# Optimization experiments

Measured on AMD Instinct MI355X. Metric: run time of the kernel, lower is better.

The kernel has to match this reference:

```python
import jax, jax.numpy as jnp
import numpy as np

B, D, N = 2, 512, 2048
H, K, V = 8, 64, 64


def setup_inputs() -> dict:
    key = jax.random.key(0)
    ks = jax.random.split(key, 5)
    scale = 0.02
    return {
        "x": jax.random.normal(ks[0], (B, D, N), dtype=jnp.float32),
        "query_proj": jax.random.normal(ks[1], (H, K, D), dtype=jnp.float32) * scale,
        "key_proj": jax.random.normal(ks[2], (D, K), dtype=jnp.float32) * scale,
        "value_proj": jax.random.normal(ks[3], (D, V), dtype=jnp.float32) * scale,
        "output_proj": jax.random.normal(ks[4], (D, H, V), dtype=jnp.float32) * scale,
    }


def reference(x, query_proj, key_proj, value_proj, output_proj):
    # x: (b, d, n); self-attention, so memory m = x as well
    key_dim = query_proj.shape[1]
    q = jnp.einsum('bdn,hkd->bnhk', x, query_proj)          # (b,n,h,k)
    k = jnp.einsum('bdm,dk->bmk', x, key_proj)              # (b,m,k) shared across heads
    v = jnp.einsum('bdm,dv->bmv', x, value_proj)            # (b,m,v) shared across heads
    sim = jnp.einsum('bnhk,bmk->bnhm', q, k) / jnp.sqrt(jnp.float32(key_dim))
    attn = jax.nn.softmax(sim, axis=-1)                     # softmax over memory dim m
    o = jnp.einsum('bnhm,bmv->bnhv', attn, v)               # (b,n,h,v)
    out = jnp.einsum('bnhv,dhv->bdn', o, output_proj)       # (b,d,n)
    return out
```

## Files before the change

kernel.cpp:

```cpp
#include <hip/hip_runtime.h>
#include <math.h>

#define BB 2
#define DDIM 512
#define NSEQ 2048
#define NHEAD 8

typedef __attribute__((ext_vector_type(4))) short s16x4;
typedef __attribute__((ext_vector_type(8))) short s16x8;
typedef __attribute__((ext_vector_type(4))) float f32x4;

__device__ __forceinline__ unsigned short f2bf(float f) {
    unsigned u = __float_as_uint(f);
    u = (u + 0x7FFFu + ((u >> 16) & 1u)) >> 16;
    return (unsigned short)u;
}
__device__ __forceinline__ float bf2f(unsigned short h) {
    return __uint_as_float(((unsigned)h) << 16);
}
__device__ __forceinline__ s16x4 pack4(float a, float b, float c, float d) {
    s16x4 r;
    r[0] = (short)f2bf(a); r[1] = (short)f2bf(b);
    r[2] = (short)f2bf(c); r[3] = (short)f2bf(d);
    return r;
}

__device__ __forceinline__ f32x4 mfma32(s16x8 a, s16x8 b, f32x4 c) {
    return __builtin_amdgcn_mfma_f32_16x16x32_bf16(a, b, c, 0, 0, 0);
}
__device__ __forceinline__ f32x4 mfma16(s16x4 a, s16x4 b, f32x4 c) {
#if __has_builtin(__builtin_amdgcn_mfma_f32_16x16x16bf16_1k)
    return __builtin_amdgcn_mfma_f32_16x16x16bf16_1k(a, b, c, 0, 0, 0);
#else
    s16x8 a8 = { a[0], a[1], a[2], a[3], 0, 0, 0, 0 };
    s16x8 b8 = { b[0], b[1], b[2], b[3], 0, 0, 0, 0 };
    return __builtin_amdgcn_mfma_f32_16x16x32_bf16(a8, b8, c, 0, 0, 0);
#endif
}

__global__ __launch_bounds__(256) void xt_kernel(
    const float* __restrict__ x, unsigned short* __restrict__ xthi,
    unsigned short* __restrict__ xtlo)
{
    __shared__ float tile[64 * 68];
    int t = threadIdx.x;
    int b = blockIdx.z, d0 = blockIdx.y * 64, n0 = blockIdx.x * 64;
    int dl = t >> 4, n4 = (t & 15) * 4;
    #pragma unroll
    for (int i = 0; i < 4; ++i) {
        int d = dl + i * 16;
        float4 v = *(const float4*)(x + ((size_t)b * DDIM + d0 + d) * NSEQ + n0 + n4);
        *(float4*)(tile + d * 68 + n4) = v;
    }
    __syncthreads();
    int nl = t >> 2, dq = (t & 3) * 16;
    size_t base = ((size_t)b * NSEQ + n0 + nl) * DDIM + d0 + dq;
    #pragma unroll
    for (int g = 0; g < 4; ++g) {
        ushort4 hv, lv;
        #pragma unroll
        for (int k = 0; k < 4; ++k) {
            float v = tile[(dq + g * 4 + k) * 68 + nl];
            unsigned short hi = f2bf(v);
            ((unsigned short*)&hv)[k] = hi;
            ((unsigned short*)&lv)[k] = f2bf(v - bf2f(hi));
        }
        *(ushort4*)(xthi + base + g * 4) = hv;
        *(ushort4*)(xtlo + base + g * 4) = lv;
    }
}

__global__ __launch_bounds__(256) void wconv_kernel(
    const float* __restrict__ qp, const float* __restrict__ op,
    unsigned short* __restrict__ qphi, unsigned short* __restrict__ qplo,
    unsigned short* __restrict__ ophi, unsigned short* __restrict__ oplo)
{
    int e = (blockIdx.x * 256 + threadIdx.x) * 4;
    const float* src = blockIdx.y ? op : qp;
    unsigned short* dh = blockIdx.y ? ophi : qphi;
    unsigned short* dl = blockIdx.y ? oplo : qplo;
    float sc = blockIdx.y ? 1.0f : 0.125f;
    float4 v = *(const float4*)(src + e);
    v.x *= sc; v.y *= sc; v.z *= sc; v.w *= sc;
    ushort4 hv, lv;
    hv.x = f2bf(v.x); lv.x = f2bf(v.x - bf2f(hv.x));
    hv.y = f2bf(v.y); lv.y = f2bf(v.y - bf2f(hv.y));
    hv.z = f2bf(v.z); lv.z = f2bf(v.z - bf2f(hv.z));
    hv.w = f2bf(v.w); lv.w = f2bf(v.w - bf2f(hv.w));
    *(ushort4*)(dh + e) = hv;
    *(ushort4*)(dl + e) = lv;
}

__global__ __launch_bounds__(256) void kvw_kernel(
    const float* __restrict__ kp, const float* __restrict__ vp,
    unsigned short* __restrict__ kpthi, unsigned short* __restrict__ kptlo,
    unsigned short* __restrict__ vpthi, unsigned short* __restrict__ vptlo)
{
    __shared__ float tile[64 * 68];
    int t = threadIdx.x;
    int d0 = blockIdx.x * 64;
    const float* src = blockIdx.y ? vp : kp;
    unsigned short* dsth = blockIdx.y ? vpthi : kpthi;
    unsigned short* dstl = blockIdx.y ? vptlo : kptlo;
    int dl = t >> 4, j4 = (t & 15) * 4;
    #pragma unroll
    for (int i = 0; i < 4; ++i) {
        int d = dl + i * 16;
        float4 v = *(const float4*)(src + (size_t)(d0 + d) * 64 + j4);
        *(float4*)(tile + d * 68 + j4) = v;
    }
    __syncthreads();
    int jl = t >> 2, dq = (t & 3) * 16;
    #pragma unroll
    for (int g = 0; g < 4; ++g) {
        ushort4 hv, lv;
        #pragma unroll
        for (int k = 0; k < 4; ++k) {
            float v = tile[(dq + g * 4 + k) * 68 + jl];
            unsigned short hi = f2bf(v);
            ((unsigned short*)&hv)[k] = hi;
            ((unsigned short*)&lv)[k] = f2bf(v - bf2f(hi));
        }
        *(ushort4*)(dsth + (size_t)jl * DDIM + d0 + dq + g * 4) = hv;
        *(ushort4*)(dstl + (size_t)jl * DDIM + d0 + dq + g * 4) = lv;
    }
}

__global__ __launch_bounds__(256, 2) void kv_proj_kernel(
    const unsigned short* __restrict__ xthi, const unsigned short* __restrict__ xtlo,
    const unsigned short* __restrict__ kpthi, const unsigned short* __restrict__ kptlo,
    const unsigned short* __restrict__ vpthi, const unsigned short* __restrict__ vptlo,
    unsigned short* __restrict__ kkhi, unsigned short* __restrict__ kklo,
    unsigned short* __restrict__ vthi, unsigned short* __restrict__ vtlo)
{
    __shared__ __align__(128) char arena[32768];
    const int tid = threadIdx.x;
    const int w = tid >> 6, l = tid & 63;
    const int qd = l >> 4, ln = l & 15;
    const int b = blockIdx.y;
    const int m0 = blockIdx.x * 64;

    const int vrow = l >> 3, gsw = (l & 7) ^ vrow;
    const int tsel = w >> 1;
    const int mhalf = (w & 1) * 32;
    const char* sxb = (const char*)(tsel ? xtlo : xthi)
        + ((size_t)(b * NSEQ + m0 + mhalf) * DDIM) * 2
        + (size_t)vrow * 1024 + (size_t)gsw * 16;
    char* dst0 = arena + tsel * 8192 + mhalf * 128;

    auto stage = [&](int buf, int s) {
        const char* gg = sxb + (size_t)s * 128;
        char* dd = dst0 + buf * 16384;
        #pragma unroll
        for (int i = 0; i < 4; ++i)
            __builtin_amdgcn_global_load_lds(
                (const __attribute__((address_space(1))) unsigned int*)(gg + (size_t)i * 8 * 1024),
                (__attribute__((address_space(3))) unsigned int*)(dd + i * 1024),
                16, 0, 0);
    };

    const int isV = w >> 1;
    const int jh  = w & 1;
    const unsigned short* wh = (isV ? vpthi : kpthi) + (size_t)(jh * 32) * DDIM;
    const unsigned short* wl = (isV ? vptlo : kptlo) + (size_t)(jh * 32) * DDIM;

    f32x4 acc[2][4];
    const f32x4 vzero = {0.f, 0.f, 0.f, 0.f};
    #pragma unroll
    for (int js = 0; js < 2; ++js)
        #pragma unroll
        for (int ms = 0; ms < 4; ++ms) acc[js][ms] = vzero;

    stage(0, 0);
    for (int s = 0; s < 8; ++s) {
        int buf = s & 1;
        __syncthreads();
        if (s + 1 < 8) stage(buf ^ 1, s + 1);
        const char* Bh = arena + buf * 16384;
        const char* Bl = Bh + 8192;
        #pragma unroll
        for (int hh = 0; hh < 2; ++hh) {
            s16x8 ah[2], al[2];
            #pragma unroll
            for (int js = 0; js < 2; ++js) {
                size_t ao = (size_t)(js * 16 + ln) * DDIM + s * 64 + hh * 32 + qd * 8;
                ah[js] = *(const s16x8*)(wh + ao);
                al[js] = *(const s16x8*)(wl + ao);
            }
            int goff = ((hh * 4 + qd) ^ (ln & 7)) * 16;
            #pragma unroll
            for (int ms = 0; ms < 4; ++ms) {
                int ro = (ms * 16 + ln) * 128 + goff;
                s16x8 bh = *(const s16x8*)(Bh + ro);
                s16x8 bl = *(const s16x8*)(Bl + ro);
                #pragma unroll
                for (int js = 0; js < 2; ++js) {
                    acc[js][ms] = mfma32(ah[js], bh, acc[js][ms]);
                    acc[js][ms] = mfma32(ah[js], bl, acc[js][ms]);
                    acc[js][ms] = mfma32(al[js], bh, acc[js][ms]);
                }
            }
        }
    }

    if (isV) {
        #pragma unroll
        for (int js = 0; js < 2; ++js)
            #pragma unroll
            for (int ms = 0; ms < 4; ++ms)
                #pragma unroll
                for (int r = 0; r < 4; ++r) {
                    int v = jh * 32 + js * 16 + qd * 4 + r;
                    size_t o = ((size_t)b * 64 + v) * NSEQ + m0 + ms * 16 + ln;
                    float val = acc[js][ms][r];
                    unsigned short hi = f2bf(val);
                    vthi[o] = hi;
                    vtlo[o] = f2bf(val - bf2f(hi));
                }
    }
    __syncthreads();
    float* eb = (float*)arena;
    if (!isV) {
        #pragma unroll
        for (int js = 0; js < 2; ++js)
            #pragma unroll
            for (int ms = 0; ms < 4; ++ms)
                #pragma unroll
                for (int r = 0; r < 4; ++r)
                    eb[(ms * 16 + ln) * 66 + jh * 32 + js * 16 + qd * 4 + r]
                        = acc[js][ms][r];
    }
    __syncthreads();
    {
        int m = tid >> 2, jg = (tid & 3) * 16;
        size_t base = ((size_t)b * NSEQ + m0 + m) * 64 + jg;
        #pragma unroll
        for (int g = 0; g < 4; ++g) {
            ushort4 hv, lv;
            #pragma unroll
            for (int k = 0; k < 4; ++k) {
                float v = eb[m * 66 + jg + g * 4 + k];
                unsigned short hi = f2bf(v);
                ((unsigned short*)&hv)[k] = hi;
                ((unsigned short*)&lv)[k] = f2bf(v - bf2f(hi));
            }
            *(ushort4*)(kkhi + base + g * 4) = hv;
            *(ushort4*)(kklo + base + g * 4) = lv;
        }
    }
}

__global__ __launch_bounds__(256, 2) void q_proj_kernel(
    const unsigned short* __restrict__ xthi, const unsigned short* __restrict__ xtlo,
    const unsigned short* __restrict__ qphi, const unsigned short* __restrict__ qplo,
    unsigned short* __restrict__ qhi, unsigned short* __restrict__ qlo)
{
    __shared__ __align__(128) char arena[65536];
    const int tid = threadIdx.x;
    const int w = tid >> 6, l = tid & 63;
    const int qd = l >> 4, ln = l & 15;
    const int b = blockIdx.z, h = blockIdx.y;
    const int n0 = blockIdx.x * 128;

    const int vrow = l >> 3, gsw = (l & 7) ^ vrow;
    const int tsel = w >> 1;
    const int rhalf = (w & 1) * 64;
    const char* sb = (const char*)(tsel ? xtlo : xthi)
        + ((size_t)(b * NSEQ + n0 + rhalf) * DDIM) * 2
        + (size_t)vrow * 1024 + (size_t)gsw * 16;
    char* dst0 = arena + tsel * 16384 + rhalf * 128;

    auto stage = [&](int buf, int s) {
        const char* gg = sb + (size_t)s * 128;
        char* dd = dst0 + buf * 32768;
        #pragma unroll
        for (int i = 0; i < 8; ++i)
            __builtin_amdgcn_global_load_lds(
                (const __attribute__((address_space(1))) unsigned int*)(gg + (size_t)i * 8192),
                (__attribute__((address_space(3))) unsigned int*)(dd + i * 1024),
                16, 0, 0);
    };

    f32x4 acc[8];
    const f32x4 vzero = {0.f, 0.f, 0.f, 0.f};
    #pragma unroll
    for (int i = 0; i < 8; ++i) acc[i] = vzero;

    const unsigned short* qpb_h = qphi + ((size_t)h * 64 + w * 16 + ln) * DDIM;
    const unsigned short* qpb_l = qplo + ((size_t)h * 64 + w * 16 + ln) * DDIM;

    stage(0, 0);
    for (int s = 0; s < 8; ++s) {
        int buf = s & 1;
        __syncthreads();
        if (s + 1 < 8) stage(buf ^ 1, s + 1);
        const char* Bh = arena + buf * 32768;
        const char* Bl = Bh + 16384;
        #pragma unroll
        for (int hh = 0; hh < 2; ++hh) {
            s16x8 ah = *(const s16x8*)(qpb_h + s * 64 + hh * 32 + qd * 8);
            s16x8 al = *(const s16x8*)(qpb_l + s * 64 + hh * 32 + qd * 8);
            int goff = ((hh * 4 + qd) ^ (ln & 7)) * 16;
            #pragma unroll
            for (int ns = 0; ns < 8; ++ns) {
                int ro = (ns * 16 + ln) * 128 + goff;
                s16x8 bh = *(const s16x8*)(Bh + ro);
                s16x8 bl = *(const s16x8*)(Bl + ro);
                acc[ns] = mfma32(ah, bh, acc[ns]);
                acc[ns] = mfma32(ah, bl, acc[ns]);
                acc[ns] = mfma32(al, bh, acc[ns]);
            }
        }
    }
    __syncthreads();
    float* eb = (float*)arena;
    #pragma unroll
    for (int ns = 0; ns < 8; ++ns)
        #pragma unroll
        for (int r = 0; r < 4; ++r)
            eb[(ns * 16 + ln) * 69 + w * 16 + qd * 4 + r] = acc[ns][r];
    __syncthreads();
    {
        int n = tid >> 1, half = tid & 1;
        size_t base = (((size_t)b * NHEAD + h) * NSEQ + n0 + n) * 64 + half * 32;
        #pragma unroll
        for (int g = 0; g < 8; ++g) {
            ushort4 hv, lv;
            #pragma unroll
            for (int k = 0; k < 4; ++k) {
                float v = eb[n * 69 + half * 32 + g * 4 + k];
                unsigned short hi = f2bf(v);
                ((unsigned short*)&hv)[k] = hi;
                ((unsigned short*)&lv)[k] = f2bf(v - bf2f(hi));
            }
            *(ushort4*)(qhi + base + g * 4) = hv;
            *(ushort4*)(qlo + base + g * 4) = lv;
        }
    }
}

__global__ __launch_bounds__(256, 2) void attn_kernel(
    const unsigned short* __restrict__ kkhi, const unsigned short* __restrict__ kklo,
    const unsigned short* __restrict__ vthi, const unsigned short* __restrict__ vtlo,
    const unsigned short* __restrict__ qhi,  const unsigned short* __restrict__ qlo,
    unsigned short* __restrict__ obfhi, unsigned short* __restrict__ obflo)
{
    __shared__ __align__(128) char arena[65536];

    const int tid = threadIdx.x;
    const int w  = tid >> 6;
    const int l  = tid & 63;
    const int qd = l >> 4;
    const int ln = l & 15;
    const int bz = blockIdx.z, hz = blockIdx.y;
    const int n0 = blockIdx.x * 64;

    s16x8 qh[4][2], qlo_[4][2];
    {
        size_t rowb = (((size_t)bz * NHEAD + hz) * NSEQ + n0 + ln) * 64 + qd * 8;
        #pragma unroll
        for (int t = 0; t < 4; ++t)
            #pragma unroll
            for (int c = 0; c < 2; ++c) {
                qh[t][c]   = *(const s16x8*)(qhi + rowb + (size_t)t * 16 * 64 + c * 32);
                qlo_[t][c] = *(const s16x8*)(qlo + rowb + (size_t)t * 16 * 64 + c * 32);
            }
    }

    const int vrow = l >> 3;
    const int gsw  = (l & 7) ^ vrow;
    const char* sb; int rs, ts;
    if      (w == 0) { sb = (const char*)kkhi; rs = 128;  ts = 8192; }
    else if (w == 1) { sb = (const char*)kklo; rs = 128;  ts = 8192; }
    else if (w == 2) { sb = (const char*)vthi; rs = 4096; ts = 128;  }
    else             { sb = (const char*)vtlo; rs = 4096; ts = 128;  }
    sb += (size_t)bz * 262144 + (size_t)vrow * rs + (size_t)gsw * 16;
    char* ldst0 = arena + w * 8192;

    auto stage = [&](int buf, int mt) {
        const char* gg = sb + (size_t)mt * ts;
        char* dst = ldst0 + buf * 32768;
        #pragma unroll
        for (int i = 0; i < 8; ++i) {
            __builtin_amdgcn_global_load_lds(
                (const __attribute__((address_space(1))) unsigned int*)(gg + (size_t)i * 8 * rs),
                (__attribute__((address_space(3))) unsigned int*)(dst + i * 1024),
                16, 0, 0);
        }
    };

    int offK[2], offV[4];
    #pragma unroll
    for (int c = 0; c < 2; ++c)
        offK[c] = (w * 16 + ln) * 128 + (((c * 4 + qd) ^ (ln & 7)) * 16);
    #pragma unroll
    for (int s = 0; s < 4; ++s)
        offV[s] = (s * 16 + ln) * 128 + (((2 * w + (qd >> 1)) ^ (ln & 7)) * 16) + (qd & 1) * 8;

    f32x4 O[4][4];
    const f32x4 vzero = {0.f, 0.f, 0.f, 0.f};
    #pragma unroll
    for (int s = 0; s < 4; ++s)
        #pragma unroll
        for (int t = 0; t < 4; ++t) O[s][t] = vzero;
    float mi[4], li[4];
    #pragma unroll
    for (int t = 0; t < 4; ++t) { mi[t] = -1e30f; li[t] = 0.f; }

    stage(0, 0);

    for (int mt = 0; mt < 32; ++mt) {
        int buf = mt & 1;
        __syncthreads();
        if (mt + 1 < 32) stage(buf ^ 1, mt + 1);
        const char* Kh = arena + buf * 32768;
        const char* Kl = Kh + 8192;
        const char* Vh = Kh + 16384;
        const char* Vl = Kh + 24576;

        s16x8 kh[2], kl[2];
        #pragma unroll
        for (int c = 0; c < 2; ++c) {
            kh[c] = *(const s16x8*)(Kh + offK[c]);
            kl[c] = *(const s16x8*)(Kl + offK[c]);
        }
        f32x4 S[4];
        #pragma unroll
        for (int t = 0; t < 4; ++t) S[t] = vzero;
        #pragma unroll
        for (int c = 0; c < 2; ++c)
            #pragma unroll
            for (int t = 0; t < 4; ++t) {
                S[t] = mfma32(kh[c], qh[t][c],   S[t]);
                S[t] = mfma32(kh[c], qlo_[t][c], S[t]);
                S[t] = mfma32(kl[c], qh[t][c],   S[t]);
            }

        s16x4 pb[4]; float corr[4];
        #pragma unroll
        for (int t = 0; t < 4; ++t) {
            float rmax = fmaxf(fmaxf(S[t][0], S[t][1]), fmaxf(S[t][2], S[t][3]));
            rmax = fmaxf(rmax, __shfl_xor(rmax, 16, 64));
            rmax = fmaxf(rmax, __shfl_xor(rmax, 32, 64));
            float mnew = fmaxf(mi[t], rmax);
            corr[t] = __expf(mi[t] - mnew);
            mi[t] = mnew;
            float p0 = __expf(S[t][0] - mnew);
            float p1 = __expf(S[t][1] - mnew);
            float p2 = __expf(S[t][2] - mnew);
            float p3 = __expf(S[t][3] - mnew);
            float ps = p0 + p1 + p2 + p3;
            ps += __shfl_xor(ps, 16, 64);
            ps += __shfl_xor(ps, 32, 64);
            li[t] = li[t] * corr[t] + ps;
            pb[t] = pack4(p0, p1, p2, p3);
        }
        #pragma unroll
        for (int s = 0; s < 4; ++s)
            #pragma unroll
            for (int t = 0; t < 4; ++t)
                O[s][t] *= corr[t];
        #pragma unroll
        for (int s = 0; s < 4; ++s) {
            s16x4 vh = *(const s16x4*)(Vh + offV[s]);
            s16x4 vl = *(const s16x4*)(Vl + offV[s]);
            #pragma unroll
            for (int t = 0; t < 4; ++t) {
                O[s][t] = mfma16(vh, pb[t], O[s][t]);
                O[s][t] = mfma16(vl, pb[t], O[s][t]);
            }
        }
    }

    float* obuf  = (float*)arena;
    float* mlm   = (float*)(arena + 4608);
    float* mll   = (float*)(arena + 5632);
    float* linvs = (float*)(arena + 6656);

    if (qd == 0) {
        #pragma unroll
        for (int t = 0; t < 4; ++t) {
            mlm[w * 64 + t * 16 + ln] = mi[t];
            mll[w * 64 + t * 16 + ln] = li[t];
        }
    }
    __syncthreads();
    float f[4];
    #pragma unroll
    for (int t = 0; t < 4; ++t) {
        float M = mlm[t * 16 + ln];
        M = fmaxf(M, mlm[64 + t * 16 + ln]);
        M = fmaxf(M, mlm[128 + t * 16 + ln]);
        M = fmaxf(M, mlm[192 + t * 16 + ln]);
        float L = 0.f;
        #pragma unroll
        for (int ww = 0; ww < 4; ++ww)
            L += mll[ww * 64 + t * 16 + ln] * __expf(mlm[ww * 64 + t * 16 + ln] - M);
        f[t] = __expf(mi[t] - M);
        if (w == 0 && qd == 0) linvs[t * 16 + ln] = 1.0f / L;
    }

    #pragma unroll
    for (int t = 0; t < 4; ++t) {
        #pragma unroll
        for (int r = 0; r < 4; ++r) {
            __syncthreads();
            #pragma unroll
            for (int s = 0; s < 4; ++s) {
                if (((w + r) & 3) == s) {
                    f32x4 val = O[s][t] * f[t];
                    float* dst = obuf + (s * 16 + qd * 4) * 17 + ln;
                    if (r == 0) {
                        dst[0]  = val[0]; dst[17] = val[1];
                        dst[34] = val[2]; dst[51] = val[3];
                    } else {
                        dst[0]  += val[0]; dst[17] += val[1];
                        dst[34] += val[2]; dst[51] += val[3];
                    }
                }
            }
        }
        __syncthreads();
        int vq = tid & 15, nl = tid >> 4;
        float il = linvs[t * 16 + nl];
        ushort4 u4h, u4l;
        #pragma unroll
        for (int k = 0; k < 4; ++k) {
            float val = obuf[(vq * 4 + k) * 17 + nl] * il;
            unsigned short hi = f2bf(val);
            ((unsigned short*)&u4h)[k] = hi;
            ((unsigned short*)&u4l)[k] = f2bf(val - bf2f(hi));
        }
        size_t off = (((size_t)bz * NSEQ + n0 + t * 16 + nl) * 512) + hz * 64 + vq * 4;
        *(ushort4*)(obfhi + off) = u4h;
        *(ushort4*)(obflo + off) = u4l;
    }
}

__global__ __launch_bounds__(256, 2) void out_proj_kernel(
    const unsigned short* __restrict__ obfhi, const unsigned short* __restrict__ obflo,
    const unsigned short* __restrict__ ophi, const unsigned short* __restrict__ oplo,
    float* __restrict__ out)
{
    __shared__ __align__(128) char arena[65536];
    const int tid = threadIdx.x;
    const int w = tid >> 6, l = tid & 63;
    const int qd = l >> 4, ln = l & 15;
    const int b = blockIdx.z, d0 = blockIdx.y * 64;
    const int n0 = blockIdx.x * 128;
    const int vrow = l >> 3, gsw = (l & 7) ^ vrow;

    const int tsel = w >> 1;
    const int rhalf = (w & 1) * 64;
    const char* sb = (const char*)(tsel ? obflo : obfhi)
        + ((size_t)(b * NSEQ + n0 + rhalf) * 512) * 2
        + (size_t)vrow * 1024 + (size_t)gsw * 16;
    char* dst0 = arena + tsel * 16384 + rhalf * 128;

    auto stage = [&](int buf, int s) {
        const char* gg = sb + (size_t)s * 128;
        char* dd = dst0 + buf * 32768;
        #pragma unroll
        for (int i = 0; i < 8; ++i)
            __builtin_amdgcn_global_load_lds(
                (const __attribute__((address_space(1))) unsigned int*)(gg + (size_t)i * 8192),
                (__attribute__((address_space(3))) unsigned int*)(dd + i * 1024),
                16, 0, 0);
    };

    f32x4 acc[8];
    const f32x4 vzero = {0.f, 0.f, 0.f, 0.f};
    #pragma unroll
    for (int i = 0; i < 8; ++i) acc[i] = vzero;

    const unsigned short* oph = ophi + (size_t)(d0 + w * 16 + ln) * 512;
    const unsigned short* opl = oplo + (size_t)(d0 + w * 16 + ln) * 512;

    stage(0, 0);
    for (int s = 0; s < 8; ++s) {
        int buf = s & 1;
        __syncthreads();
        if (s + 1 < 8) stage(buf ^ 1, s + 1);
        const char* Bh = arena + buf * 32768;
        const char* Bl = Bh + 16384;
        #pragma unroll
        for (int hh = 0; hh < 2; ++hh) {
            s16x8 ah = *(const s16x8*)(oph + s * 64 + hh * 32 + qd * 8);
            s16x8 al = *(const s16x8*)(opl + s * 64 + hh * 32 + qd * 8);
            int goff = ((hh * 4 + qd) ^ (ln & 7)) * 16;
            #pragma unroll
            for (int ns = 0; ns < 8; ++ns) {
                int ro = (ns * 16 + ln) * 128 + goff;
                s16x8 bh = *(const s16x8*)(Bh + ro);
                s16x8 bl = *(const s16x8*)(Bl + ro);
                acc[ns] = mfma32(ah, bh, acc[ns]);
                acc[ns] = mfma32(ah, bl, acc[ns]);
                acc[ns] = mfma32(al, bh, acc[ns]);
            }
        }
    }
    #pragma unroll
    for (int ns = 0; ns < 8; ++ns)
        #pragma unroll
        for (int r = 0; r < 4; ++r)
            out[((size_t)b * DDIM + d0 + w * 16 + qd * 4 + r) * NSEQ
                + n0 + ns * 16 + ln] = acc[ns][r];
}

extern "C" void kernel_launch(void* const* d_in, const int* in_sizes, int n_in,
                              void* d_out, int out_size, void* d_ws, size_t ws_size,
                              hipStream_t stream) {
    const float* x  = (const float*)d_in[0];
    const float* qp = (const float*)d_in[1];
    const float* kp = (const float*)d_in[2];
    const float* vp = (const float*)d_in[3];
    const float* op = (const float*)d_in[4];
    float* out = (float*)d_out;

    unsigned short* ws    = (unsigned short*)d_ws;
    unsigned short* kkhi  = ws;
    unsigned short* kklo  = kkhi + 262144;
    unsigned short* vthi  = kklo + 262144;
    unsigned short* vtlo  = vthi + 262144;
    unsigned short* qphi  = vtlo + 262144;
    unsigned short* qplo  = qphi + 262144;
    unsigned short* ophi  = qplo + 262144;
    unsigned short* oplo  = ophi + 262144;
    unsigned short* kpthi = oplo + 262144;
    unsigned short* kptlo = kpthi + 32768;
    unsigned short* vpthi = kptlo + 32768;
    unsigned short* vptlo = vpthi + 32768;
    unsigned short* xthi  = vptlo + 32768;
    unsigned short* xtlo  = xthi + 2097152;
    unsigned short* qhi   = xtlo + 2097152;
    unsigned short* qlo   = qhi + 2097152;
    unsigned short* obfhi = xthi;
    unsigned short* obflo = xtlo;

    hipLaunchKernelGGL(xt_kernel,       dim3(32, 8, 2),  dim3(256), 0, stream,
                       x, xthi, xtlo);
    hipLaunchKernelGGL(wconv_kernel,    dim3(256, 2),    dim3(256), 0, stream,
                       qp, op, qphi, qplo, ophi, oplo);
    hipLaunchKernelGGL(kvw_kernel,      dim3(8, 2),      dim3(256), 0, stream,
                       kp, vp, kpthi, kptlo, vpthi, vptlo);
    hipLaunchKernelGGL(kv_proj_kernel,  dim3(32, 2),     dim3(256), 0, stream,
                       xthi, xtlo, kpthi, kptlo, vpthi, vptlo,
                       kkhi, kklo, vthi, vtlo);
    hipLaunchKernelGGL(q_proj_kernel,   dim3(16, 8, 2),  dim3(256), 0, stream,
                       xthi, xtlo, qphi, qplo, qhi, qlo);
    hipLaunchKernelGGL(attn_kernel,     dim3(32, 8, 2),  dim3(256), 0, stream,
                       kkhi, kklo, vthi, vtlo, qhi, qlo, obfhi, obflo);
    hipLaunchKernelGGL(out_proj_kernel, dim3(16, 8, 2),  dim3(256), 0, stream,
                       obfhi, obflo, ophi, oplo, out);
}
```

Measured before the change: 192.9 us.

## Load K fragments directly from global into registers, stage only V in LDS

Each wave now reads its private K tile slice straight from global memory into registers, prefetching the next tile after the QK MFMAs, instead of staging K through shared memory. Only the V tiles still go through LDS, and all four waves share that load, so the LDS arena shrinks from 64KB to 32KB. This is meant to cut LDS traffic and footprint and possibly allow more resident blocks. In exchange the K loads become uncoalesced per-lane global reads whose latency must hide behind the softmax and PV work. A barrier is added before the epilogue reuses the arena.

Result: no change. 194.6 us (+0.9%).

```diff
diff --git a/kernel.cpp b/kernel.cpp
--- a/kernel.cpp
+++ b/kernel.cpp
@@ -345,7 +345,7 @@
     const unsigned short* __restrict__ qhi,  const unsigned short* __restrict__ qlo,
     unsigned short* __restrict__ obfhi, unsigned short* __restrict__ obflo)
 {
-    __shared__ __align__(128) char arena[65536];
+    __shared__ __align__(128) char arena[32768];
 
     const int tid = threadIdx.x;
     const int w  = tid >> 6;
@@ -369,30 +369,29 @@
 
     const int vrow = l >> 3;
     const int gsw  = (l & 7) ^ vrow;
-    const char* sb; int rs, ts;
-    if      (w == 0) { sb = (const char*)kkhi; rs = 128;  ts = 8192; }
-    else if (w == 1) { sb = (const char*)kklo; rs = 128;  ts = 8192; }
-    else if (w == 2) { sb = (const char*)vthi; rs = 4096; ts = 128;  }
-    else             { sb = (const char*)vtlo; rs = 4096; ts = 128;  }
-    sb += (size_t)bz * 262144 + (size_t)vrow * rs + (size_t)gsw * 16;
-    char* ldst0 = arena + w * 8192;
+    const char* sb = (const char*)(w < 2 ? vthi : vtlo)
+        + (size_t)bz * 262144
+        + (size_t)((w & 1) * 32 + vrow) * 4096 + (size_t)gsw * 16;
+    char* dst0 = arena + (w >> 1) * 8192 + (w & 1) * 4096;
 
     auto stage = [&](int buf, int mt) {
-        const char* gg = sb + (size_t)mt * ts;
-        char* dst = ldst0 + buf * 32768;
-        #pragma unroll
-        for (int i = 0; i < 8; ++i) {
+        const char* gg = sb + (size_t)mt * 128;
+        char* dst = dst0 + buf * 16384;
+        #pragma unroll
+        for (int i = 0; i < 4; ++i) {
             __builtin_amdgcn_global_load_lds(
-                (const __attribute__((address_space(1))) unsigned int*)(gg + (size_t)i * 8 * rs),
+                (const __attribute__((address_space(1))) unsigned int*)(gg + (size_t)i * 8 * 4096),
                 (__attribute__((address_space(3))) unsigned int*)(dst + i * 1024),
                 16, 0, 0);
         }
     };
 
-    int offK[2], offV[4];
-    #pragma unroll
-    for (int c = 0; c < 2; ++c)
-        offK[c] = (w * 16 + ln) * 128 + (((c * 4 + qd) ^ (ln & 7)) * 16);
+    const char* kH = (const char*)kkhi + (size_t)bz * 262144
+        + (size_t)(w * 16 + ln) * 128 + qd * 16;
+    const char* kL = (const char*)kklo + (size_t)bz * 262144
+        + (size_t)(w * 16 + ln) * 128 + qd * 16;
+
+    int offV[4];
     #pragma unroll
     for (int s = 0; s < 4; ++s)
         offV[s] = (s * 16 + ln) * 128 + (((2 * w + (qd >> 1)) ^ (ln & 7)) * 16) + (qd & 1) * 8;
@@ -408,22 +407,20 @@
     for (int t = 0; t < 4; ++t) { mi[t] = -1e30f; li[t] = 0.f; }
 
     stage(0, 0);
+    s16x8 kh[2], kl[2];
+    #pragma unroll
+    for (int c = 0; c < 2; ++c) {
+        kh[c] = *(const s16x8*)(kH + c * 64);
+        kl[c] = *(const s16x8*)(kL + c * 64);
+    }
 
     for (int mt = 0; mt < 32; ++mt) {
         int buf = mt & 1;
         __syncthreads();
         if (mt + 1 < 32) stage(buf ^ 1, mt + 1);
-        const char* Kh = arena + buf * 32768;
-        const char* Kl = Kh + 8192;
-        const char* Vh = Kh + 16384;
-        const char* Vl = Kh + 24576;
-
-        s16x8 kh[2], kl[2];
-        #pragma unroll
-        for (int c = 0; c < 2; ++c) {
-            kh[c] = *(const s16x8*)(Kh + offK[c]);
-            kl[c] = *(const s16x8*)(Kl + offK[c]);
-        }
+        const char* Vh = arena + buf * 16384;
+        const char* Vl = Vh + 8192;
+
         f32x4 S[4];
         #pragma unroll
         for (int t = 0; t < 4; ++t) S[t] = vzero;
@@ -435,6 +432,13 @@
                 S[t] = mfma32(kh[c], qlo_[t][c], S[t]);
                 S[t] = mfma32(kl[c], qh[t][c],   S[t]);
             }
+        if (mt + 1 < 32) {
+            #pragma unroll
+            for (int c = 0; c < 2; ++c) {
+                kh[c] = *(const s16x8*)(kH + (size_t)(mt + 1) * 8192 + c * 64);
+                kl[c] = *(const s16x8*)(kL + (size_t)(mt + 1) * 8192 + c * 64);
+            }
+        }
 
         s16x4 pb[4]; float corr[4];
         #pragma unroll
@@ -477,6 +481,7 @@
     float* mll   = (float*)(arena + 5632);
     float* linvs = (float*)(arena + 6656);
 
+    __syncthreads();
     if (qd == 0) {
         #pragma unroll
         for (int t = 0; t < 4; ++t) {
```
